# Kernel optimization log

Measured on AMD Instinct MI355X. Metric: run time of the kernel, lower is better.

The kernel has to match this reference:

```python
import jax, jax.numpy as jnp
import numpy as np

B, D = 8192, 128
MARGIN = 0.1
N_CLASSES, N_GROUPS = 64, 8


def setup_inputs() -> dict:
    key = jax.random.key(0)
    k1, k2, k3 = jax.random.split(key, 3)
    embeddings = jax.random.normal(k1, (B, D), dtype=jnp.float32)
    labels = jax.random.randint(k2, (B,), 0, N_CLASSES, dtype=jnp.int64)
    groups = jax.random.randint(k3, (B,), 0, N_GROUPS, dtype=jnp.int64)
    return {"embeddings": embeddings, "labels": labels, "groups": groups}


def reference(embeddings, labels, groups):
    # cosine metric: L2-normalize rows (torch F.normalize eps=1e-12)
    norm = jnp.maximum(jnp.linalg.norm(embeddings, axis=1, keepdims=True), 1e-12)
    x = embeddings / norm
    dist = 1.0 - jnp.matmul(x, x.T)                      # [B, B]

    n = embeddings.shape[0]
    eye = jnp.eye(n, dtype=bool)
    same_label = labels[:, None] == labels[None, :]       # [B, B]
    pos_mask = same_label & ~eye
    neg_mask = ~same_label
    neg_sg_mask = neg_mask & (groups[:, None] == groups[None, :])

    BIG = jnp.float32(1e9)
    # hardest positive per row (masked max), hardest negative per row (masked min)
    dist_ap = jnp.max(jnp.where(pos_mask, dist, -BIG), axis=1)
    dist_an_sg = jnp.min(jnp.where(neg_sg_mask, dist, BIG), axis=1)
    dist_an_all = jnp.min(jnp.where(neg_mask, dist, BIG), axis=1)

    has_pos = jnp.any(pos_mask, axis=1)
    has_neg_sg = jnp.any(neg_sg_mask, axis=1)
    has_neg = jnp.any(neg_mask, axis=1)

    # fallback: same-group negatives preferred, else any negative
    dist_an = jnp.where(has_neg_sg, dist_an_sg, dist_an_all)

    loss = jax.nn.relu(dist_ap - dist_an + MARGIN)        # [B]
    # original only averages strictly-positive losses over valid anchors
    include = has_pos & has_neg & (loss > 0)
    cnt = jnp.sum(include.astype(jnp.float32))
    total = jnp.sum(jnp.where(include, loss, 0.0))
    final = jnp.where(cnt > 0, total / jnp.maximum(cnt, 1.0), 0.0)
    final = jnp.where(jnp.isnan(final), 0.0, final)
    return final
```

## Files before the change

kernel.cpp:

```cpp
#include <hip/hip_runtime.h>
#include <math.h>

#define NB 8192
#define DK 128
#define IT 128
#define JT 64
#define SPLITJ 16
#define JSPAN (NB / SPLITJ)
#define NT (JSPAN / JT)
#define BSTRH 136
#define NCOMB (NB / 256)

typedef __attribute__((ext_vector_type(8))) short short8;
typedef __attribute__((ext_vector_type(16))) float float16;

__device__ inline unsigned short f2bf(float f) {
    unsigned int x = __float_as_uint(f);
    unsigned int r = (x + 0x7fffu + ((x >> 16) & 1u)) >> 16;
    return (unsigned short)r;
}

__global__ void norm_kernel(const float* __restrict__ emb, const int* __restrict__ labels,
                            const int* __restrict__ groups, unsigned short* __restrict__ xnb,
                            int* __restrict__ meta) {
    int row  = blockIdx.x * 4 + (threadIdx.x >> 6);
    int lane = threadIdx.x & 63;
    float2 v = ((const float2*)(emb + (size_t)row * DK))[lane];
    float ss = v.x * v.x + v.y * v.y;
#pragma unroll
    for (int off = 32; off; off >>= 1) ss += __shfl_xor(ss, off, 64);
    float inv = 1.0f / fmaxf(sqrtf(ss), 1e-12f);
    ushort2 o;
    o.x = f2bf(v.x * inv);
    o.y = f2bf(v.y * inv);
    ((ushort2*)(xnb + (size_t)row * DK))[lane] = o;
    if (lane == 0) meta[row] = (labels[row] << 8) | groups[row];
}

__global__ __launch_bounds__(256, 3) void mine_mfma(
    const unsigned short* __restrict__ xnb, const int* __restrict__ meta,
    float* __restrict__ ap_part, float* __restrict__ an_part) {
    __shared__ unsigned short Bs[2][JT * BSTRH];

    const int tid  = threadIdx.x;
    const int w    = tid >> 6;
    const int lane = tid & 63;
    const int half = lane >> 5;
    const int l31  = lane & 31;
    const int i0    = blockIdx.x * IT;
    const int jbase = blockIdx.y * JSPAN;
    const int irow  = i0 + w * 32;

    short8 afrag[8];
#pragma unroll
    for (int ks = 0; ks < 8; ks++)
        afrag[ks] = *(const short8*)(xnb + (size_t)(irow + l31) * DK + ks * 16 + half * 8);

    int metaI[16];
    float apn[16], anc[16];
#pragma unroll
    for (int reg = 0; reg < 16; reg++) {
        int r = (reg & 3) + 8 * (reg >> 2) + 4 * half;
        metaI[reg] = meta[irow + r];
        apn[reg] = -1e9f; anc[reg] = -1e9f;
    }

#pragma unroll
    for (int s = 0; s < 4; s++) {
        int chunk = tid + s * 256;
        int row = chunk >> 4, k4 = chunk & 15;
        *(uint4*)&Bs[0][row * BSTRH + k4 * 8] =
            *(const uint4*)(xnb + (size_t)(jbase + row) * DK + k4 * 8);
    }
    __syncthreads();

    for (int jt = 0; jt < NT; jt++) {
        const int cur = jt & 1;
        const int j0  = jbase + jt * JT;

        uint4 pre[4];
        if (jt + 1 < NT) {
            const int j0n = j0 + JT;
#pragma unroll
            for (int s = 0; s < 4; s++) {
                int chunk = tid + s * 256;
                int row = chunk >> 4, k4 = chunk & 15;
                pre[s] = *(const uint4*)(xnb + (size_t)(j0n + row) * DK + k4 * 8);
            }
        }

        int mjc[2];
        mjc[0] = meta[j0 + l31];
        mjc[1] = meta[j0 + 32 + l31];

#pragma unroll
        for (int ct = 0; ct < 2; ct++) {
            float16 c;
#pragma unroll
            for (int e = 0; e < 16; e++) c[e] = 0.0f;

            const int bro = ct * 32 + l31;
#pragma unroll
            for (int ks = 0; ks < 8; ks++) {
                short8 b = *(const short8*)&Bs[cur][bro * BSTRH + ks * 16 + half * 8];
                c = __builtin_amdgcn_mfma_f32_32x32x16_bf16(afrag[ks], b, c, 0, 0, 0);
            }

            const int mj = mjc[ct];
#pragma unroll
            for (int reg = 0; reg < 16; reg++) {
                float s = c[reg];
                int x = metaI[reg] ^ mj;
                bool sl = (unsigned)x < 0x100u;
                float t8 = s - 8.0f;
                float t  = sl ? t8 : s;
                apn[reg] = fmaxf(apn[reg], -t);
                bool sg = (x & 0xFFu) == 0u;
                float t4 = t + 4.0f;
                float v  = sg ? t4 : t;
                anc[reg] = fmaxf(anc[reg], v);
            }
        }

        if (jt + 1 < NT) {
#pragma unroll
            for (int s = 0; s < 4; s++) {
                int chunk = tid + s * 256;
                int row = chunk >> 4, k4 = chunk & 15;
                *(uint4*)&Bs[cur ^ 1][row * BSTRH + k4 * 8] = pre[s];
            }
        }
        __syncthreads();
    }

#pragma unroll
    for (int reg = 0; reg < 16; reg++) {
#pragma unroll
        for (int off = 16; off; off >>= 1) {
            apn[reg] = fmaxf(apn[reg], __shfl_xor(apn[reg], off, 64));
            anc[reg] = fmaxf(anc[reg], __shfl_xor(anc[reg], off, 64));
        }
    }
    if (l31 == 0) {
#pragma unroll
        for (int reg = 0; reg < 16; reg++) {
            int r = (reg & 3) + 8 * (reg >> 2) + 4 * half;
            size_t idx = (size_t)blockIdx.y * NB + (irow + r);
            ap_part[idx] = apn[reg];
            an_part[idx] = anc[reg];
        }
    }
}

__global__ void combine_kernel(const float* __restrict__ ap_part,
                               const float* __restrict__ an_part,
                               float* __restrict__ accum, int* __restrict__ ticket,
                               float* __restrict__ out) {
    int i = blockIdx.x * 256 + threadIdx.x;
    float apn = -1e9f, anc = -1e9f;
#pragma unroll
    for (int h = 0; h < SPLITJ; h++) {
        size_t idx = (size_t)h * NB + i;
        apn = fmaxf(apn, ap_part[idx]);
        anc = fmaxf(anc, an_part[idx]);
    }
    float anS = (anc > 2.0f) ? anc - 4.0f : anc;
    float loss = anS + apn - 7.9f;
    float inc = (loss > 0.0f) ? 1.0f : 0.0f;
    float val = inc * loss;

    __shared__ float ssum[4], scnt[4];
#pragma unroll
    for (int off = 32; off; off >>= 1) {
        val += __shfl_xor(val, off, 64);
        inc += __shfl_xor(inc, off, 64);
    }
    int wid = threadIdx.x >> 6, lane = threadIdx.x & 63;
    if (lane == 0) { ssum[wid] = val; scnt[wid] = inc; }
    __syncthreads();
    if (threadIdx.x == 0) {
        float s = 0.f, c = 0.f;
#pragma unroll
        for (int wv = 0; wv < 4; wv++) { s += ssum[wv]; c += scnt[wv]; }
        atomicAdd(&accum[0], s);
        atomicAdd(&accum[1], c);
        __threadfence();
        int old = atomicAdd(ticket, 1);
        if (old == gridDim.x - 1) {
            __threadfence();
            float total = __hip_atomic_load(&accum[0], __ATOMIC_RELAXED, __HIP_MEMORY_SCOPE_AGENT);
            float cnt   = __hip_atomic_load(&accum[1], __ATOMIC_RELAXED, __HIP_MEMORY_SCOPE_AGENT);
            float r = (cnt > 0.0f) ? total / fmaxf(cnt, 1.0f) : 0.0f;
            if (isnan(r)) r = 0.0f;
            out[0] = r;
        }
    }
}

extern "C" void kernel_launch(void* const* d_in, const int* in_sizes, int n_in,
                              void* d_out, int out_size, void* d_ws, size_t ws_size,
                              hipStream_t stream) {
    const float* emb  = (const float*)d_in[0];
    const int* labels = (const int*)d_in[1];
    const int* groups = (const int*)d_in[2];
    float* out = (float*)d_out;

    unsigned short* xnb = (unsigned short*)d_ws;
    int*   meta    = (int*)(xnb + (size_t)NB * DK);
    float* ap_part = (float*)(meta + NB);
    float* an_part = ap_part + (size_t)SPLITJ * NB;
    float* accum   = an_part + (size_t)SPLITJ * NB;
    int*   ticket  = (int*)(accum + 2);

    hipMemsetAsync(accum, 0, 3 * sizeof(float), stream);
    norm_kernel<<<NB / 4, 256, 0, stream>>>(emb, labels, groups, xnb, meta);
    mine_mfma<<<dim3(NB / IT, SPLITJ), 256, 0, stream>>>(
        xnb, meta, ap_part, an_part);
    combine_kernel<<<NCOMB, 256, 0, stream>>>(ap_part, an_part, accum, ticket, out);
}
```

Baseline: 99.51 us.

## Exploit symmetric distance matrix by computing only upper-triangular tiles

The mining kernel now launches one block per upper-triangular 128x128 tile pair. Each block reduces its tile both per row and per column, since dist is symmetric, which roughly halves the MFMA work. The combine kernel merges the row partials and the column partials for each anchor. The memset is also folded into the norm kernel. In exchange, each block covers a much shorter j span (two 64-wide subtiles) and so pays more fixed setup, it needs an extra LDS column reduction, and the combine kernel reads more partial data.

```diff
diff --git a/kernel.cpp b/kernel.cpp
--- a/kernel.cpp
+++ b/kernel.cpp
@@ -3,11 +3,11 @@
 
 #define NB 8192
 #define DK 128
-#define IT 128
+#define TI 128
+#define NTILES (NB / TI)
+#define NBLK (NTILES * (NTILES + 1) / 2)
 #define JT 64
-#define SPLITJ 16
-#define JSPAN (NB / SPLITJ)
-#define NT (JSPAN / JT)
+#define NT (TI / JT)
 #define BSTRH 136
 #define NCOMB (NB / 256)
 
@@ -22,7 +22,8 @@
 
 __global__ void norm_kernel(const float* __restrict__ emb, const int* __restrict__ labels,
                             const int* __restrict__ groups, unsigned short* __restrict__ xnb,
-                            int* __restrict__ meta) {
+                            int* __restrict__ meta, float* __restrict__ accum,
+                            int* __restrict__ ticket) {
     int row  = blockIdx.x * 4 + (threadIdx.x >> 6);
     int lane = threadIdx.x & 63;
     float2 v = ((const float2*)(emb + (size_t)row * DK))[lane];
@@ -35,20 +36,29 @@
     o.y = f2bf(v.y * inv);
     ((ushort2*)(xnb + (size_t)row * DK))[lane] = o;
     if (lane == 0) meta[row] = (labels[row] << 8) | groups[row];
-}
-
-__global__ __launch_bounds__(256, 3) void mine_mfma(
+    if (blockIdx.x == 0 && threadIdx.x == 0) {
+        accum[0] = 0.0f; accum[1] = 0.0f; ticket[0] = 0;
+    }
+}
+
+__global__ __launch_bounds__(256, 3) void mine_tri(
     const unsigned short* __restrict__ xnb, const int* __restrict__ meta,
-    float* __restrict__ ap_part, float* __restrict__ an_part) {
+    float* __restrict__ ap_row, float* __restrict__ an_row,
+    float* __restrict__ ap_col, float* __restrict__ an_col) {
     __shared__ unsigned short Bs[2][JT * BSTRH];
+
+    int bid = blockIdx.x;
+    int ti = 0;
+    while (bid >= NTILES - ti) { bid -= NTILES - ti; ti++; }
+    const int tj = ti + bid;
 
     const int tid  = threadIdx.x;
     const int w    = tid >> 6;
     const int lane = tid & 63;
     const int half = lane >> 5;
     const int l31  = lane & 31;
-    const int i0    = blockIdx.x * IT;
-    const int jbase = blockIdx.y * JSPAN;
+    const int i0    = ti * TI;
+    const int jbase = tj * TI;
     const int irow  = i0 + w * 32;
 
     short8 afrag[8];
@@ -64,6 +74,9 @@
         metaI[reg] = meta[irow + r];
         apn[reg] = -1e9f; anc[reg] = -1e9f;
     }
+    float apnC[4], ancC[4];
+#pragma unroll
+    for (int q = 0; q < 4; q++) { apnC[q] = -1e9f; ancC[q] = -1e9f; }
 
 #pragma unroll
     for (int s = 0; s < 4; s++) {
@@ -74,6 +87,7 @@
     }
     __syncthreads();
 
+#pragma unroll
     for (int jt = 0; jt < NT; jt++) {
         const int cur = jt & 1;
         const int j0  = jbase + jt * JT;
@@ -107,6 +121,7 @@
             }
 
             const int mj = mjc[ct];
+            const int q  = jt * 2 + ct;
 #pragma unroll
             for (int reg = 0; reg < 16; reg++) {
                 float s = c[reg];
@@ -114,11 +129,14 @@
                 bool sl = (unsigned)x < 0x100u;
                 float t8 = s - 8.0f;
                 float t  = sl ? t8 : s;
-                apn[reg] = fmaxf(apn[reg], -t);
+                float negt = -t;
+                apn[reg] = fmaxf(apn[reg], negt);
+                apnC[q]  = fmaxf(apnC[q],  negt);
                 bool sg = (x & 0xFFu) == 0u;
                 float t4 = t + 4.0f;
                 float v  = sg ? t4 : t;
                 anc[reg] = fmaxf(anc[reg], v);
+                ancC[q]  = fmaxf(ancC[q],  v);
             }
         }
 
@@ -145,24 +163,54 @@
 #pragma unroll
         for (int reg = 0; reg < 16; reg++) {
             int r = (reg & 3) + 8 * (reg >> 2) + 4 * half;
-            size_t idx = (size_t)blockIdx.y * NB + (irow + r);
-            ap_part[idx] = apn[reg];
-            an_part[idx] = anc[reg];
-        }
-    }
-}
-
-__global__ void combine_kernel(const float* __restrict__ ap_part,
-                               const float* __restrict__ an_part,
+            size_t idx = (size_t)tj * NB + (irow + r);
+            ap_row[idx] = apn[reg];
+            an_row[idx] = anc[reg];
+        }
+    }
+
+    float* colred = (float*)&Bs[0][0];
+#pragma unroll
+    for (int q = 0; q < 4; q++) {
+        apnC[q] = fmaxf(apnC[q], __shfl_xor(apnC[q], 32, 64));
+        ancC[q] = fmaxf(ancC[q], __shfl_xor(ancC[q], 32, 64));
+        if (half == 0) {
+            colred[0 * 512 + w * 128 + q * 32 + l31] = apnC[q];
+            colred[1 * 512 + w * 128 + q * 32 + l31] = ancC[q];
+        }
+    }
+    __syncthreads();
+    {
+        int arr = tid >> 7;
+        int e   = tid & 127;
+        float m = -1e9f;
+#pragma unroll
+        for (int wv = 0; wv < 4; wv++)
+            m = fmaxf(m, colred[arr * 512 + wv * 128 + e]);
+        size_t idx = (size_t)ti * NB + (jbase + e);
+        if (arr == 0) ap_col[idx] = m;
+        else          an_col[idx] = m;
+    }
+}
+
+__global__ void combine_kernel(const float* __restrict__ ap_row,
+                               const float* __restrict__ an_row,
+                               const float* __restrict__ ap_col,
+                               const float* __restrict__ an_col,
                                float* __restrict__ accum, int* __restrict__ ticket,
                                float* __restrict__ out) {
     int i = blockIdx.x * 256 + threadIdx.x;
+    int ti = i >> 7;
     float apn = -1e9f, anc = -1e9f;
-#pragma unroll
-    for (int h = 0; h < SPLITJ; h++) {
-        size_t idx = (size_t)h * NB + i;
-        apn = fmaxf(apn, ap_part[idx]);
-        anc = fmaxf(anc, an_part[idx]);
+    for (int s = ti; s < NTILES; s++) {
+        size_t idx = (size_t)s * NB + i;
+        apn = fmaxf(apn, ap_row[idx]);
+        anc = fmaxf(anc, an_row[idx]);
+    }
+    for (int s = 0; s <= ti; s++) {
+        size_t idx = (size_t)s * NB + i;
+        apn = fmaxf(apn, ap_col[idx]);
+        anc = fmaxf(anc, an_col[idx]);
     }
     float anS = (anc > 2.0f) ? anc - 4.0f : anc;
     float loss = anS + apn - 7.9f;
@@ -206,15 +254,15 @@
     float* out = (float*)d_out;
 
     unsigned short* xnb = (unsigned short*)d_ws;
-    int*   meta    = (int*)(xnb + (size_t)NB * DK);
-    float* ap_part = (float*)(meta + NB);
-    float* an_part = ap_part + (size_t)SPLITJ * NB;
-    float* accum   = an_part + (size_t)SPLITJ * NB;
-    int*   ticket  = (int*)(accum + 2);
-
-    hipMemsetAsync(accum, 0, 3 * sizeof(float), stream);
-    norm_kernel<<<NB / 4, 256, 0, stream>>>(emb, labels, groups, xnb, meta);
-    mine_mfma<<<dim3(NB / IT, SPLITJ), 256, 0, stream>>>(
-        xnb, meta, ap_part, an_part);
-    combine_kernel<<<NCOMB, 256, 0, stream>>>(ap_part, an_part, accum, ticket, out);
-}
+    int*   meta   = (int*)(xnb + (size_t)NB * DK);
+    float* ap_row = (float*)(meta + NB);
+    float* an_row = ap_row + (size_t)NTILES * NB;
+    float* ap_col = an_row + (size_t)NTILES * NB;
+    float* an_col = ap_col + (size_t)NTILES * NB;
+    float* accum  = an_col + (size_t)NTILES * NB;
+    int*   ticket = (int*)(accum + 2);
+
+    norm_kernel<<<NB / 4, 256, 0, stream>>>(emb, labels, groups, xnb, meta, accum, ticket);
+    mine_tri<<<NBLK, 256, 0, stream>>>(xnb, meta, ap_row, an_row, ap_col, an_col);
+    combine_kernel<<<NCOMB, 256, 0, stream>>>(ap_row, an_row, ap_col, an_col, accum, ticket, out);
+}
```

Measured after the change: 115.0 us. 15.5% more time.
